# Kernel tuning notes

Measured on AMD Instinct MI355X. Metric: run time of the kernel, lower is better.

## Reference

```python
import jax, jax.numpy as jnp
import numpy as np

B, S, F = 8, 1024, 512
E, H = 64, 16  # embed_dim per head, n_heads (match init_kwargs)


def setup_inputs() -> dict:
    key = jax.random.key(0)
    k1, k2, k3, k4, k5, k6 = jax.random.split(key, 6)
    inputs1 = jax.random.normal(k1, (B, S, F), dtype=jnp.float32)
    inputs2 = jax.random.normal(k2, (B, S, F), dtype=jnp.float32)
    W_kv = jax.random.normal(k3, (F, E * H * 2), dtype=jnp.float32) * 0.02
    b_kv = jax.random.normal(k4, (E * H * 2,), dtype=jnp.float32) * 0.02
    W_q = jax.random.normal(k5, (F, E * H), dtype=jnp.float32) * 0.02
    b_q = jax.random.normal(k6, (E * H,), dtype=jnp.float32) * 0.02
    return {"inputs1": inputs1, "inputs2": inputs2,
            "W_kv": W_kv, "b_kv": b_kv, "W_q": W_q, "b_q": b_q}


def reference(inputs1, inputs2, W_kv, b_kv, W_q, b_q):
    scaling = 1.0 / jnp.sqrt(jnp.float32(E))
    # KV path: Dense then reshape (B,S,E,H,2) -> transpose to (B,2,H,S,E)
    kv = inputs1 @ W_kv + b_kv                      # (B,S,E*H*2), layout d-major
    kv = kv.reshape(B, S, E, H, 2)
    kv = jnp.transpose(kv, (0, 4, 3, 1, 2))        # (B,2,H,S,E)
    k = kv[:, 0]                                   # (B,H,S,E)
    v = kv[:, 1]                                   # (B,H,S,E)
    # Q path: Dense then reshape (B,S,E,H) -> (B,H,S,E)
    q = (inputs2 @ W_q + b_q).reshape(B, S, E, H)
    q = jnp.transpose(q, (0, 3, 1, 2))             # (B,H,S,E)
    # Attention: softmax FIRST, then scale (non-standard, faithful to source)
    qk = jnp.einsum('bhqe,bhke->bhqk', q, k)       # (B,H,S,S)
    attn = jax.nn.softmax(qk, axis=-1) * scaling
    out = jnp.einsum('bhqk,bhke->bhqe', attn, v)   # (B,H,S,E)
    out = jnp.transpose(out, (0, 2, 1, 3))         # (B,S,H,E)
    return out.reshape(B, S, E * H)
```

## Files before the change

### kernel.cpp

```cpp
#include <hip/hip_runtime.h>
#include <hip/hip_bf16.h>
#include <math.h>

#define NB 8
#define NS 1024
#define NF 512
#define NE 64
#define NH 16

typedef __attribute__((ext_vector_type(8))) short short8;
typedef __attribute__((ext_vector_type(4))) float floatx4;

__device__ inline unsigned short f2bf(float f) {
  union { float f; unsigned int u; } c; c.f = f;
  unsigned int u = c.u;
  u += 0x7FFFu + ((u >> 16) & 1u);
  return (unsigned short)(u >> 16);
}

__device__ inline unsigned int cvt_pk_bf16(float a, float b) {
  unsigned int r;
  asm("v_cvt_pk_bf16_f32 %0, %1, %2" : "=v"(r) : "v"(a), "v"(b));
  return r;
}

__device__ inline float fexp2(float x) {
#if __has_builtin(__builtin_amdgcn_exp2f)
  return __builtin_amdgcn_exp2f(x);
#else
  return exp2f(x);
#endif
}

__device__ inline void gl_lds16(const void* g, void* l) {
  __builtin_amdgcn_global_load_lds(
      (const __attribute__((address_space(1))) unsigned int*)g,
      (__attribute__((address_space(3))) unsigned int*)l, 16, 0, 0);
}

__global__ __launch_bounds__(256) void conv_bf16_dual(
    const float* __restrict__ in1, const float* __restrict__ in2,
    unsigned short* __restrict__ out1, unsigned short* __restrict__ out2, int n4)
{
  const float* in = blockIdx.y ? in2 : in1;
  unsigned short* out = blockIdx.y ? out2 : out1;
  int i = blockIdx.x * 256 + threadIdx.x;
  if (i < n4) {
    float4 v = ((const float4*)in)[i];
    ushort4 o;
    o.x = f2bf(v.x); o.y = f2bf(v.y); o.z = f2bf(v.z); o.w = f2bf(v.w);
    ((ushort4*)out)[i] = o;
  }
}

template <int LOGG>
__global__ __launch_bounds__(256) void perm_w(
    const float* __restrict__ W, unsigned short* __restrict__ Wt, int N)
{
  __shared__ float T[64][65];
  const int t = threadIdx.x;
  const int k0 = blockIdx.y * 64, n0 = blockIdx.x * 64;
  #pragma unroll
  for (int p = 0; p < 4; ++p) {
    int i = (t >> 4) + p * 16, j = (t & 15) * 4;
    float4 v = *(const float4*)(W + (size_t)(k0 + i) * N + n0 + j);
    T[i][j] = v.x; T[i][j + 1] = v.y; T[i][j + 2] = v.z; T[i][j + 3] = v.w;
  }
  __syncthreads();
  #pragma unroll
  for (int p = 0; p < 2; ++p) {
    int c = p * 256 + t;
    int jn = c >> 3, kc = (c & 7) * 8;
    int n = n0 + jn;
    int g = n & ((1 << LOGG) - 1), e = n >> LOGG;
    unsigned short v[8];
    #pragma unroll
    for (int j = 0; j < 8; ++j) v[j] = f2bf(T[kc + j][jn]);
    *(uint4*)(Wt + (size_t)(g * 64 + e) * NF + k0 + kc) = *(uint4*)v;
  }
}

template <int MODE>
__global__ __launch_bounds__(256) void gemm_proj(
    const unsigned short* __restrict__ A, const unsigned short* __restrict__ Wt,
    const float* __restrict__ bias, unsigned short* __restrict__ out0,
    unsigned short* __restrict__ out1)
{
  __shared__ union {
    struct { unsigned short A[2][128 * 32]; unsigned short B[2][128 * 32]; } ab;
    unsigned short C[128 * 136];
    struct { unsigned short K[128][72]; unsigned short V[64][136]; } kv;
  } u;

  const int t = threadIdx.x;
  const int w = t >> 6, l = t & 63;
  const int quad = l >> 4, l16 = l & 15;
  const int NX = (MODE == 0) ? 16 : 8;
  const int nwg = NX * 64;
  const int bid = blockIdx.x;
  const int swz = (bid & 7) * (nwg >> 3) + (bid >> 3);
  const int n0 = (swz % NX) * 128, m0 = (swz / NX) * 128;
  const int wm = (w >> 1) * 64, wn = (w & 1) * 64;

  floatx4 acc[4][4];
  #pragma unroll
  for (int mi = 0; mi < 4; ++mi)
    #pragma unroll
    for (int nj = 0; nj < 4; ++nj) acc[mi][nj] = (floatx4){0.f, 0.f, 0.f, 0.f};

  const unsigned short* Ag = A + (size_t)(m0 + w * 16 + (l >> 2)) * NF + (l & 3) * 8;
  const unsigned short* Bg = Wt + (size_t)(n0 + w * 16 + (l >> 2)) * NF + (l & 3) * 8;

  gl_lds16(Ag,           &u.ab.A[0][(w * 16) * 32]);
  gl_lds16(Ag + 64 * NF, &u.ab.A[0][(64 + w * 16) * 32]);
  gl_lds16(Bg,           &u.ab.B[0][(w * 16) * 32]);
  gl_lds16(Bg + 64 * NF, &u.ab.B[0][(64 + w * 16) * 32]);

  for (int kt = 0; kt < 16; ++kt) {
    __syncthreads();
    const int cur = kt & 1;
    if (kt < 15) {
      const int k0 = (kt + 1) * 32;
      gl_lds16(Ag + k0,           &u.ab.A[cur ^ 1][(w * 16) * 32]);
      gl_lds16(Ag + 64 * NF + k0, &u.ab.A[cur ^ 1][(64 + w * 16) * 32]);
      gl_lds16(Bg + k0,           &u.ab.B[cur ^ 1][(w * 16) * 32]);
      gl_lds16(Bg + 64 * NF + k0, &u.ab.B[cur ^ 1][(64 + w * 16) * 32]);
    }
    short8 af[4], bf[4];
    #pragma unroll
    for (int mi = 0; mi < 4; ++mi)
      af[mi] = *(const short8*)&u.ab.A[cur][(wm + mi * 16 + l16) * 32 + quad * 8];
    #pragma unroll
    for (int nj = 0; nj < 4; ++nj)
      bf[nj] = *(const short8*)&u.ab.B[cur][(wn + nj * 16 + l16) * 32 + quad * 8];
    #pragma unroll
    for (int mi = 0; mi < 4; ++mi)
      #pragma unroll
      for (int nj = 0; nj < 4; ++nj)
        acc[mi][nj] = __builtin_amdgcn_mfma_f32_16x16x32_bf16(
            af[mi], bf[nj], acc[mi][nj], 0, 0, 0);
  }

  float bv[4];
  #pragma unroll
  for (int nj = 0; nj < 4; ++nj) {
    int np = n0 + wn + nj * 16 + l16;
    int n = (MODE == 0) ? ((np & 63) * 32 + (np >> 6)) : ((np & 63) * 16 + (np >> 6));
    bv[nj] = bias[n];
  }
  __syncthreads();

  if (MODE == 0) {
    if (wn == 0) {
      #pragma unroll
      for (int mi = 0; mi < 4; ++mi)
        #pragma unroll
        for (int nj = 0; nj < 4; ++nj)
          #pragma unroll
          for (int r = 0; r < 4; ++r)
            u.kv.K[wm + mi * 16 + quad * 4 + r][nj * 16 + l16] =
                f2bf(acc[mi][nj][r] + bv[nj]);
    } else {
      #pragma unroll
      for (int mi = 0; mi < 4; ++mi)
        #pragma unroll
        for (int nj = 0; nj < 4; ++nj)
          #pragma unroll
          for (int r = 0; r < 4; ++r)
            u.kv.V[nj * 16 + l16][wm + mi * 16 + quad * 4 + r] =
                f2bf(acc[mi][nj][r] + bv[nj]);
    }
  } else {
    const float LOG2E = 1.44269504088896f;
    #pragma unroll
    for (int mi = 0; mi < 4; ++mi)
      #pragma unroll
      for (int nj = 0; nj < 4; ++nj)
        #pragma unroll
        for (int r = 0; r < 4; ++r)
          u.C[(wm + mi * 16 + quad * 4 + r) * 136 + wn + nj * 16 + l16] =
              f2bf((acc[mi][nj][r] + bv[nj]) * LOG2E);
  }
  __syncthreads();

  if (MODE == 0) {
    const int h = n0 >> 7, btile = m0 >> 10, s0 = m0 & 1023;
    #pragma unroll
    for (int p = 0; p < 4; ++p) {
      int c = p * 256 + t;
      int m = c >> 3, ec = c & 7;
      uint4 v = *(const uint4*)&u.kv.K[m][ec * 8];
      *(uint4*)(out0 + (((size_t)btile * NH + h) * NS + s0 + m) * NE + ec * 8) = v;
    }
    #pragma unroll
    for (int p = 0; p < 4; ++p) {
      int c = p * 256 + t;
      int e = c >> 4, mc = c & 15;
      uint4 v = *(const uint4*)&u.kv.V[e][mc * 8];
      *(uint4*)(out1 + (((size_t)btile * NH + h) * NE + e) * NS + s0 + mc * 8) = v;
    }
  } else {
    #pragma unroll
    for (int p = 0; p < 8; ++p) {
      int c = p * 256 + t;
      int m = c >> 4, col8 = (c & 15) * 8;
      uint4 v = *(const uint4*)&u.C[m * 136 + col8];
      int mg = m0 + m, b = mg >> 10, s = mg & 1023;
      int h = (n0 >> 6) + (col8 >> 6), e0 = col8 & 63;
      *(uint4*)(out0 + (((size_t)b * NH + h) * NS + s) * NE + e0) = v;
    }
  }
}

__global__ __launch_bounds__(256, 2) void attn_kernel(
    const unsigned short* __restrict__ Q, const unsigned short* __restrict__ K,
    const unsigned short* __restrict__ Vt, float* __restrict__ out)
{
  __shared__ unsigned short Ks[2][64][64];
  __shared__ unsigned short Vs[2][64][64];

  const int t = threadIdx.x;
  const int w = t >> 6, lane = t & 63;
  const int quad = lane >> 4, l16 = lane & 15;
  const int n = blockIdx.x;
  const int qt = n >> 7;
  const int g = n & 127;
  const int h = g & 15, b = g >> 4;
  const size_t bh = ((size_t)b * NH + h) * NS * NE;
  const int q0 = qt * 256 + w * 64;

  short8 aq[4][2];
  #pragma unroll
  for (int rb = 0; rb < 4; ++rb) {
    const unsigned short* qrow = Q + bh + (size_t)(q0 + rb * 16 + l16) * NE;
    aq[rb][0] = *(const short8*)(qrow + quad * 8);
    aq[rb][1] = *(const short8*)(qrow + 32 + quad * 8);
  }

  const int sr = t >> 3, sc8 = t & 7;
  const int xs = (sc8 ^ (sr & 7)) * 8;
  const int xq = (quad ^ (l16 & 7)) * 8;
  const unsigned short* Kg = K + bh;
  const unsigned short* Vg = Vt + bh;

  {
    *(uint4*)&Ks[0][sr][xs]      = *(const uint4*)(Kg + (size_t)sr * NE + sc8 * 8);
    *(uint4*)&Ks[0][32 + sr][xs] = *(const uint4*)(Kg + (size_t)(32 + sr) * NE + sc8 * 8);
    *(uint4*)&Vs[0][sr][xs]      = *(const uint4*)(Vg + (size_t)sr * NS + sc8 * 8);
    *(uint4*)&Vs[0][32 + sr][xs] = *(const uint4*)(Vg + (size_t)(32 + sr) * NS + sc8 * 8);
  }

  float lsum[4] = {0.f, 0.f, 0.f, 0.f};
  floatx4 O[4][4];
  #pragma unroll
  for (int rb = 0; rb < 4; ++rb)
    #pragma unroll
    for (int j = 0; j < 4; ++j) O[rb][j] = (floatx4){0.f, 0.f, 0.f, 0.f};

  for (int kt = 0; kt < NS / 64; ++kt) {
    __syncthreads();
    const int bi = kt & 1;

    uint4 kn0, kn1, vn0, vn1;
    if (kt < 15) {
      const unsigned short* kg = Kg + (size_t)(kt + 1) * 64 * NE;
      kn0 = *(const uint4*)(kg + (size_t)sr * NE + sc8 * 8);
      kn1 = *(const uint4*)(kg + (size_t)(32 + sr) * NE + sc8 * 8);
      const unsigned short* vg = Vg + (kt + 1) * 64;
      vn0 = *(const uint4*)(vg + (size_t)sr * NS + sc8 * 8);
      vn1 = *(const uint4*)(vg + (size_t)(32 + sr) * NS + sc8 * 8);
    }

    short8 kf0[4], kf1[4];
    #pragma unroll
    for (int kb = 0; kb < 4; ++kb) {
      kf0[kb] = *(const short8*)&Ks[bi][kb * 16 + l16][xq];
      kf1[kb] = *(const short8*)&Ks[bi][kb * 16 + l16][xq ^ 32];
    }

    short8 paf[4][2];
    #pragma unroll
    for (int rb = 0; rb < 4; ++rb) {
      floatx4 st[4];
      __builtin_amdgcn_s_setprio(1);
      #pragma unroll
      for (int kb = 0; kb < 4; ++kb) {
        floatx4 z = (floatx4){0.f, 0.f, 0.f, 0.f};
        z = __builtin_amdgcn_mfma_f32_16x16x32_bf16(kf0[kb], aq[rb][0], z, 0, 0, 0);
        st[kb] = __builtin_amdgcn_mfma_f32_16x16x32_bf16(kf1[kb], aq[rb][1], z, 0, 0, 0);
      }
      __builtin_amdgcn_s_setprio(0);
      unsigned int c[4][2];
      #pragma unroll
      for (int kb = 0; kb < 4; ++kb) {
        float p0 = fexp2(st[kb][0]), p1 = fexp2(st[kb][1]);
        float p2 = fexp2(st[kb][2]), p3 = fexp2(st[kb][3]);
        lsum[rb] += (p0 + p1) + (p2 + p3);
        c[kb][0] = cvt_pk_bf16(p0, p1);
        c[kb][1] = cvt_pk_bf16(p2, p3);
      }
      #pragma unroll
      for (int m = 0; m < 2; ++m) {
        union { unsigned int wd[4]; short8 v; } pu;
        #pragma unroll
        for (int j = 0; j < 2; ++j) {
          unsigned int a = c[2 * m][j], bb = c[2 * m + 1][j];
          asm("v_permlane32_swap_b32 %0, %1" : "+v"(a), "+v"(bb));
          asm("v_permlane16_swap_b32 %0, %1" : "+v"(a), "+v"(bb));
          pu.wd[j]     = a;
          pu.wd[2 + j] = bb;
        }
        paf[rb][m] = pu.v;
      }
    }

    short8 vf0[4], vf1[4];
    #pragma unroll
    for (int eb = 0; eb < 4; ++eb) {
      vf0[eb] = *(const short8*)&Vs[bi][eb * 16 + l16][xq];
      vf1[eb] = *(const short8*)&Vs[bi][eb * 16 + l16][xq ^ 32];
    }
    __builtin_amdgcn_s_setprio(1);
    #pragma unroll
    for (int rb = 0; rb < 4; ++rb) {
      #pragma unroll
      for (int eb = 0; eb < 4; ++eb) {
        O[rb][eb] = __builtin_amdgcn_mfma_f32_16x16x32_bf16(paf[rb][0], vf0[eb], O[rb][eb], 0, 0, 0);
        O[rb][eb] = __builtin_amdgcn_mfma_f32_16x16x32_bf16(paf[rb][1], vf1[eb], O[rb][eb], 0, 0, 0);
      }
    }
    __builtin_amdgcn_s_setprio(0);

    if (kt < 15) {
      const int bn = bi ^ 1;
      *(uint4*)&Ks[bn][sr][xs]      = kn0;
      *(uint4*)&Ks[bn][32 + sr][xs] = kn1;
      *(uint4*)&Vs[bn][sr][xs]      = vn0;
      *(uint4*)&Vs[bn][32 + sr][xs] = vn1;
    }
  }

  const float scaling = 0.125f;
  #pragma unroll
  for (int rb = 0; rb < 4; ++rb) {
    float lv = lsum[rb];
    lv += __shfl_xor(lv, 16);
    lv += __shfl_xor(lv, 32);
    #pragma unroll
    for (int r = 0; r < 4; ++r) {
      float inv = scaling / __shfl(lv, quad * 4 + r);
      int s = q0 + rb * 16 + quad * 4 + r;
      float* orow = out + ((size_t)b * NS + s) * (NE * NH) + h * NE;
      orow[l16]      = O[rb][0][r] * inv;
      orow[16 + l16] = O[rb][1][r] * inv;
      orow[32 + l16] = O[rb][2][r] * inv;
      orow[48 + l16] = O[rb][3][r] * inv;
    }
  }
}

extern "C" void kernel_launch(void* const* d_in, const int* in_sizes, int n_in,
                              void* d_out, int out_size, void* d_ws, size_t ws_size,
                              hipStream_t stream) {
  const float* inputs1 = (const float*)d_in[0];
  const float* inputs2 = (const float*)d_in[1];
  const float* W_kv    = (const float*)d_in[2];
  const float* b_kv    = (const float*)d_in[3];
  const float* W_q     = (const float*)d_in[4];
  const float* b_q     = (const float*)d_in[5];
  float* out = (float*)d_out;

  const size_t plane = (size_t)NB * NH * NS * NE;
  const size_t amat  = (size_t)NB * NS * NF;
  unsigned short* Qb   = (unsigned short*)d_ws;
  unsigned short* Kb   = Qb + plane;
  unsigned short* Vtb  = Kb + plane;
  unsigned short* A1b  = Vtb + plane;
  unsigned short* A2b  = A1b + amat;
  unsigned short* Wtkv = A2b + amat;
  unsigned short* Wtq  = Wtkv + (size_t)2048 * NF;

  dim3 blk(256);
  conv_bf16_dual<<<dim3(amat / 4 / 256, 2), blk, 0, stream>>>(
      inputs1, inputs2, A1b, A2b, amat / 4);
  perm_w<5><<<dim3(2048 / 64, NF / 64), blk, 0, stream>>>(W_kv, Wtkv, 2048);
  perm_w<4><<<dim3(1024 / 64, NF / 64), blk, 0, stream>>>(W_q, Wtq, 1024);
  gemm_proj<0><<<dim3(1024), blk, 0, stream>>>(A1b, Wtkv, b_kv, Kb, Vtb);
  gemm_proj<1><<<dim3(512), blk, 0, stream>>>(A2b, Wtq, b_q, Qb, nullptr);
  attn_kernel<<<dim3(512), blk, 0, stream>>>(Qb, Kb, Vtb, out);
}
```

Measured before the change: 98.54 us.

## Fuse fp32-to-bf16 activation conversion into projection GEMM and merge launches

Removes the separate activation conversion kernel. The GEMM now loads fp32 activations directly, packs them to bf16 in registers and writes them to LDS. The two weight-permute kernels are merged into one launch, and the KV and Q projection GEMMs are merged into a single grid of 1536 blocks. This cuts three launches and the bf16 activation write/read round trip, but the A-operand path loses async global-to-LDS loads and now reads twice as many bytes per tile through registers, which may expose load latency in the GEMM main loop.

```diff
diff --git a/kernel.cpp b/kernel.cpp
--- a/kernel.cpp
+++ b/kernel.cpp
@@ -38,28 +38,20 @@
       (__attribute__((address_space(3))) unsigned int*)l, 16, 0, 0);
 }
 
-__global__ __launch_bounds__(256) void conv_bf16_dual(
-    const float* __restrict__ in1, const float* __restrict__ in2,
-    unsigned short* __restrict__ out1, unsigned short* __restrict__ out2, int n4)
-{
-  const float* in = blockIdx.y ? in2 : in1;
-  unsigned short* out = blockIdx.y ? out2 : out1;
-  int i = blockIdx.x * 256 + threadIdx.x;
-  if (i < n4) {
-    float4 v = ((const float4*)in)[i];
-    ushort4 o;
-    o.x = f2bf(v.x); o.y = f2bf(v.y); o.z = f2bf(v.z); o.w = f2bf(v.w);
-    ((ushort4*)out)[i] = o;
-  }
-}
-
-template <int LOGG>
-__global__ __launch_bounds__(256) void perm_w(
-    const float* __restrict__ W, unsigned short* __restrict__ Wt, int N)
+__global__ __launch_bounds__(256) void perm_w_dual(
+    const float* __restrict__ Wkv, const float* __restrict__ Wq,
+    unsigned short* __restrict__ Wtkv, unsigned short* __restrict__ Wtq)
 {
   __shared__ float T[64][65];
   const int t = threadIdx.x;
-  const int k0 = blockIdx.y * 64, n0 = blockIdx.x * 64;
+  const int k0 = blockIdx.y * 64;
+  const int bx = blockIdx.x;
+  const float* W;
+  unsigned short* Wt;
+  int N, n0, logg;
+  if (bx < 32) { W = Wkv; Wt = Wtkv; N = 2048; n0 = bx * 64; logg = 5; }
+  else         { W = Wq;  Wt = Wtq;  N = 1024; n0 = (bx - 32) * 64; logg = 4; }
+
   #pragma unroll
   for (int p = 0; p < 4; ++p) {
     int i = (t >> 4) + p * 16, j = (t & 15) * 4;
@@ -72,7 +64,7 @@
     int c = p * 256 + t;
     int jn = c >> 3, kc = (c & 7) * 8;
     int n = n0 + jn;
-    int g = n & ((1 << LOGG) - 1), e = n >> LOGG;
+    int g = n & ((1 << logg) - 1), e = n >> logg;
     unsigned short v[8];
     #pragma unroll
     for (int j = 0; j < 8; ++j) v[j] = f2bf(T[kc + j][jn]);
@@ -80,24 +72,23 @@
   }
 }
 
+union GemmLds {
+  struct { unsigned short A[2][128 * 32]; unsigned short B[2][128 * 32]; } ab;
+  unsigned short C[128 * 136];
+  struct { unsigned short K[128][72]; unsigned short V[64][136]; } kv;
+};
+
 template <int MODE>
-__global__ __launch_bounds__(256) void gemm_proj(
-    const unsigned short* __restrict__ A, const unsigned short* __restrict__ Wt,
+__device__ __forceinline__ void gemm_body(
+    const float* __restrict__ A32, const unsigned short* __restrict__ Wt,
     const float* __restrict__ bias, unsigned short* __restrict__ out0,
-    unsigned short* __restrict__ out1)
+    unsigned short* __restrict__ out1, GemmLds& u, int bid)
 {
-  __shared__ union {
-    struct { unsigned short A[2][128 * 32]; unsigned short B[2][128 * 32]; } ab;
-    unsigned short C[128 * 136];
-    struct { unsigned short K[128][72]; unsigned short V[64][136]; } kv;
-  } u;
-
   const int t = threadIdx.x;
   const int w = t >> 6, l = t & 63;
   const int quad = l >> 4, l16 = l & 15;
   const int NX = (MODE == 0) ? 16 : 8;
   const int nwg = NX * 64;
-  const int bid = blockIdx.x;
   const int swz = (bid & 7) * (nwg >> 3) + (bid >> 3);
   const int n0 = (swz % NX) * 128, m0 = (swz / NX) * 128;
   const int wm = (w >> 1) * 64, wn = (w & 1) * 64;
@@ -108,11 +99,23 @@
     #pragma unroll
     for (int nj = 0; nj < 4; ++nj) acc[mi][nj] = (floatx4){0.f, 0.f, 0.f, 0.f};
 
-  const unsigned short* Ag = A + (size_t)(m0 + w * 16 + (l >> 2)) * NF + (l & 3) * 8;
+  const float* Ag = A32 + (size_t)(m0 + w * 16 + (l >> 2)) * NF + (l & 3) * 8;
   const unsigned short* Bg = Wt + (size_t)(n0 + w * 16 + (l >> 2)) * NF + (l & 3) * 8;
 
-  gl_lds16(Ag,           &u.ab.A[0][(w * 16) * 32]);
-  gl_lds16(Ag + 64 * NF, &u.ab.A[0][(64 + w * 16) * 32]);
+  auto stageA = [&](int buf, int k0) {
+    #pragma unroll
+    for (int hf = 0; hf < 2; ++hf) {
+      const float* src = Ag + (size_t)hf * 64 * NF + k0;
+      float4 fa = *(const float4*)src;
+      float4 fb = *(const float4*)(src + 4);
+      uint4 pk;
+      pk.x = cvt_pk_bf16(fa.x, fa.y); pk.y = cvt_pk_bf16(fa.z, fa.w);
+      pk.z = cvt_pk_bf16(fb.x, fb.y); pk.w = cvt_pk_bf16(fb.z, fb.w);
+      *(uint4*)&u.ab.A[buf][(hf * 64 + w * 16 + (l >> 2)) * 32 + (l & 3) * 8] = pk;
+    }
+  };
+
+  stageA(0, 0);
   gl_lds16(Bg,           &u.ab.B[0][(w * 16) * 32]);
   gl_lds16(Bg + 64 * NF, &u.ab.B[0][(64 + w * 16) * 32]);
 
@@ -121,8 +124,7 @@
     const int cur = kt & 1;
     if (kt < 15) {
       const int k0 = (kt + 1) * 32;
-      gl_lds16(Ag + k0,           &u.ab.A[cur ^ 1][(w * 16) * 32]);
-      gl_lds16(Ag + 64 * NF + k0, &u.ab.A[cur ^ 1][(64 + w * 16) * 32]);
+      stageA(cur ^ 1, k0);
       gl_lds16(Bg + k0,           &u.ab.B[cur ^ 1][(w * 16) * 32]);
       gl_lds16(Bg + 64 * NF + k0, &u.ab.B[cur ^ 1][(64 + w * 16) * 32]);
     }
@@ -210,6 +212,19 @@
       *(uint4*)(out0 + (((size_t)b * NH + h) * NS + s) * NE + e0) = v;
     }
   }
+}
+
+__global__ __launch_bounds__(256) void gemm_fused(
+    const float* __restrict__ in1, const float* __restrict__ in2,
+    const unsigned short* __restrict__ Wtkv, const unsigned short* __restrict__ Wtq,
+    const float* __restrict__ b_kv, const float* __restrict__ b_q,
+    unsigned short* __restrict__ Kb, unsigned short* __restrict__ Vtb,
+    unsigned short* __restrict__ Qb)
+{
+  __shared__ GemmLds u;
+  const int bid = blockIdx.x;
+  if (bid < 1024) gemm_body<0>(in1, Wtkv, b_kv, Kb, Vtb, u, bid);
+  else            gemm_body<1>(in2, Wtq,  b_q,  Qb, nullptr, u, bid - 1024);
 }
 
 __global__ __launch_bounds__(256, 2) void attn_kernel(
@@ -371,21 +386,15 @@
   float* out = (float*)d_out;
 
   const size_t plane = (size_t)NB * NH * NS * NE;
-  const size_t amat  = (size_t)NB * NS * NF;
   unsigned short* Qb   = (unsigned short*)d_ws;
   unsigned short* Kb   = Qb + plane;
   unsigned short* Vtb  = Kb + plane;
-  unsigned short* A1b  = Vtb + plane;
-  unsigned short* A2b  = A1b + amat;
-  unsigned short* Wtkv = A2b + amat;
+  unsigned short* Wtkv = Vtb + plane;
   unsigned short* Wtq  = Wtkv + (size_t)2048 * NF;
 
   dim3 blk(256);
-  conv_bf16_dual<<<dim3(amat / 4 / 256, 2), blk, 0, stream>>>(
-      inputs1, inputs2, A1b, A2b, amat / 4);
-  perm_w<5><<<dim3(2048 / 64, NF / 64), blk, 0, stream>>>(W_kv, Wtkv, 2048);
-  perm_w<4><<<dim3(1024 / 64, NF / 64), blk, 0, stream>>>(W_q, Wtq, 1024);
-  gemm_proj<0><<<dim3(1024), blk, 0, stream>>>(A1b, Wtkv, b_kv, Kb, Vtb);
-  gemm_proj<1><<<dim3(512), blk, 0, stream>>>(A2b, Wtq, b_q, Qb, nullptr);
+  perm_w_dual<<<dim3(48, NF / 64), blk, 0, stream>>>(W_kv, W_q, Wtkv, Wtq);
+  gemm_fused<<<dim3(1536), blk, 0, stream>>>(
+      inputs1, inputs2, Wtkv, Wtq, b_kv, b_q, Kb, Vtb, Qb);
   attn_kernel<<<dim3(512), blk, 0, stream>>>(Qb, Kb, Vtb, out);
 }
```

New measurement: 95.39 us. 1.03x faster.
